# Kernel optimization log

Measured on AMD Instinct MI355X. Metric: run time of the kernel, lower is better.

## Reference

```python
import jax, jax.numpy as jnp
import numpy as np

N_NODES = 100000
N_EDGES = 1280000
IN_DIM = 64
OUT_DIM = 64


def setup_inputs() -> dict:
    key = jax.random.key(0)
    k1, k2, k3, k4, k5 = jax.random.split(key, 5)
    features = jax.random.normal(k1, (N_NODES, IN_DIM), dtype=jnp.float32)
    w = jax.random.uniform(k2, (N_EDGES,), dtype=jnp.float32)
    # torch nn.Linear weight is [out, in]; we store it as [in, out] so h @ W
    W = jax.random.normal(k3, (IN_DIM, OUT_DIM), dtype=jnp.float32) * (1.0 / np.sqrt(IN_DIM))
    src = jax.random.randint(k4, (N_EDGES,), 0, N_NODES, dtype=jnp.int64 if jax.config.jax_enable_x64 else jnp.int32)
    dst = jax.random.randint(k5, (N_EDGES,), 0, N_NODES, dtype=jnp.int64 if jax.config.jax_enable_x64 else jnp.int32)
    return {"features": features, "w": w, "W": W, "src": src, "dst": dst}


def reference(features, w, W, src, dst):
    num_nodes = features.shape[0]
    # u_mul_e: per-edge message = h[src] * w  (edge-weighted SpMM gather-multiply)
    msg = features[src] * w[:, None]                     # [E, in_dim]
    # fn.sum('m','h'): scatter-add messages to destination nodes
    agg = jax.ops.segment_sum(msg, dst, num_segments=num_nodes)  # [N, in_dim]
    # D_in = 1 / clamp(in_degree, min=1)
    deg = jax.ops.segment_sum(jnp.ones_like(w), dst, num_segments=num_nodes)
    d_in = 1.0 / jnp.maximum(deg, 1.0)                   # [N]
    h = agg * d_in[:, None]
    # linear (bias=False), activation None, batch_norm False, dropout 0
    return h @ W                                         # [N, out_dim]
```

## Files before the change

kernel.cpp:

```cpp
#include <hip/hip_runtime.h>

#define N_NODES 100000
#define N_EDGES 1280000
#define DIM 64
#define NBINS 391
#define CAP 3712
#define EPB 4096
#define NFB 313
#define CONVB 512
#define WSCALE (1.0f / 32767.0f)

__device__ __forceinline__ unsigned bf16_rne(float x) {
    unsigned u = __float_as_uint(x);
    return (u + 0x7fffu + ((u >> 16) & 1u)) >> 16;
}
__device__ __forceinline__ float rl_f(float v, int l) {
    return __int_as_float(__builtin_amdgcn_readlane(__float_as_int(v), l));
}
__device__ __forceinline__ float bf_lo(unsigned q) { return __uint_as_float(q << 16); }
__device__ __forceinline__ float bf_hi(unsigned q) { return __uint_as_float(q & 0xffff0000u); }

__global__ __launch_bounds__(256) void k_fill_conv(
    const int* __restrict__ src, const float* __restrict__ w,
    const int* __restrict__ dst, int* __restrict__ cursor,
    uint2* __restrict__ binned,
    const float* __restrict__ feat, const float* __restrict__ W,
    unsigned short* __restrict__ fW) {
    __shared__ int h[NBINS];
    __shared__ int base_[NBINS];
    int t = threadIdx.x;

    if (blockIdx.x < NFB) {
        for (int i = t; i < NBINS; i += 256) h[i] = 0;
        __syncthreads();
        int eb = blockIdx.x * EPB;
        int d[16], sv[16];
        unsigned wq[16];
        #pragma unroll
        for (int j = 0; j < 16; ++j) {
            int e = eb + j * 256 + t;
            if (e < N_EDGES) {
                d[j] = dst[e];
                sv[j] = src[e];
                wq[j] = (unsigned)(w[e] * 32767.0f + 0.5f);
                atomicAdd(&h[d[j] >> 8], 1);
            } else d[j] = -1;
        }
        __syncthreads();
        for (int i = t; i < NBINS; i += 256) {
            int c = h[i];
            base_[i] = c ? atomicAdd(&cursor[i], c) : 0;
            h[i] = 0;
        }
        __syncthreads();
        #pragma unroll
        for (int j = 0; j < 16; ++j) {
            if (d[j] >= 0) {
                int bin = d[j] >> 8;
                int pos = base_[bin] + atomicAdd(&h[bin], 1);
                binned[bin * CAP + pos] =
                    make_uint2((unsigned)sv[j] | ((unsigned)(d[j] & 255) << 17), wq[j]);
            }
        }
    } else {
        int lane = t & 63;
        float wcol[DIM];
        #pragma unroll
        for (int k = 0; k < DIM; ++k) wcol[k] = W[k * DIM + lane];
        int wave = ((blockIdx.x - NFB) * 256 + t) >> 6;
        int nw = CONVB * 4;
        for (int n0 = wave; n0 < N_NODES; n0 += 2 * nw) {
            int n1 = n0 + nw;
            float ha = feat[n0 * DIM + lane];
            float hb = (n1 < N_NODES) ? feat[n1 * DIM + lane] : 0.f;
            float a0 = 0, a1 = 0, a2 = 0, a3 = 0, b0 = 0, b1 = 0, b2 = 0, b3 = 0;
            #pragma unroll
            for (int k = 0; k < DIM; k += 4) {
                a0 = fmaf(rl_f(ha, k + 0), wcol[k + 0], a0);
                a1 = fmaf(rl_f(ha, k + 1), wcol[k + 1], a1);
                a2 = fmaf(rl_f(ha, k + 2), wcol[k + 2], a2);
                a3 = fmaf(rl_f(ha, k + 3), wcol[k + 3], a3);
                b0 = fmaf(rl_f(hb, k + 0), wcol[k + 0], b0);
                b1 = fmaf(rl_f(hb, k + 1), wcol[k + 1], b1);
                b2 = fmaf(rl_f(hb, k + 2), wcol[k + 2], b2);
                b3 = fmaf(rl_f(hb, k + 3), wcol[k + 3], b3);
            }
            fW[n0 * DIM + lane] = (unsigned short)bf16_rne((a0 + a1) + (a2 + a3));
            if (n1 < N_NODES)
                fW[n1 * DIM + lane] = (unsigned short)bf16_rne((b0 + b1) + (b2 + b3));
        }
    }
}

__global__ __launch_bounds__(256) void k_sortbin(const uint2* __restrict__ binned,
                                                 const int* __restrict__ cursor,
                                                 unsigned* __restrict__ csrp,
                                                 int* __restrict__ offs,
                                                 int* __restrict__ cnt) {
    __shared__ int h[256];
    __shared__ int excl[256];
    __shared__ unsigned stage[CAP];
    int b = blockIdx.x, t = threadIdx.x;
    int total = cursor[b];
    int segbase = b * CAP;
    h[t] = 0;
    __syncthreads();
    for (int i = t; i < total; i += 256)
        atomicAdd(&h[(binned[segbase + i].x >> 17) & 255], 1);
    __syncthreads();
    int v = h[t];
    excl[t] = v;
    __syncthreads();
    for (int off = 1; off < 256; off <<= 1) {
        int add = (t >= off) ? excl[t - off] : 0;
        __syncthreads();
        excl[t] += add;
        __syncthreads();
    }
    int ex = excl[t] - v;
    excl[t] = ex;
    int node = (b << 8) + t;
    if (node < N_NODES) { cnt[node] = v; offs[node] = segbase + ex; }
    h[t] = 0;
    __syncthreads();
    for (int i = t; i < total; i += 256) {
        uint2 e = binned[segbase + i];
        int o = (e.x >> 17) & 255;
        int pos = excl[o] + atomicAdd(&h[o], 1);
        if (pos < CAP) stage[pos] = (e.x & 0x1ffffu) | (e.y << 17);
    }
    __syncthreads();
    for (int i = t; i < total; i += 256)
        csrp[segbase + i] = stage[i];
}

__global__ __launch_bounds__(256) void k_gather(const uint4* __restrict__ fW4,
                                                const unsigned* __restrict__ csrp,
                                                const int* __restrict__ offs,
                                                const int* __restrict__ cnt,
                                                float* __restrict__ out) {
    int lane = threadIdx.x & 63;
    int g = lane >> 3, s = lane & 7;
    int wave = (blockIdx.x * 256 + threadIdx.x) >> 6;
    int nw = gridDim.x * 4;

    for (int node = wave; node < N_NODES; node += nw) {
        int start = offs[node];
        int c = cnt[node];
        int end = start + c;
        float a[8] = {0, 0, 0, 0, 0, 0, 0, 0};
        for (int i = start; i < end; i += 16) {
            int i0 = i + g, i1 = i + 8 + g;
            unsigned p0 = csrp[(i0 < end) ? i0 : start];
            unsigned p1 = csrp[(i1 < end) ? i1 : start];
            float w0 = (i0 < end) ? (float)(p0 >> 17) * WSCALE : 0.f;
            float w1 = (i1 < end) ? (float)(p1 >> 17) * WSCALE : 0.f;
            uint4 q0 = fW4[((p0 & 0x1ffffu) << 3) + s];
            uint4 q1 = fW4[((p1 & 0x1ffffu) << 3) + s];
            a[0] = fmaf(bf_lo(q0.x), w0, a[0]); a[1] = fmaf(bf_hi(q0.x), w0, a[1]);
            a[2] = fmaf(bf_lo(q0.y), w0, a[2]); a[3] = fmaf(bf_hi(q0.y), w0, a[3]);
            a[4] = fmaf(bf_lo(q0.z), w0, a[4]); a[5] = fmaf(bf_hi(q0.z), w0, a[5]);
            a[6] = fmaf(bf_lo(q0.w), w0, a[6]); a[7] = fmaf(bf_hi(q0.w), w0, a[7]);
            a[0] = fmaf(bf_lo(q1.x), w1, a[0]); a[1] = fmaf(bf_hi(q1.x), w1, a[1]);
            a[2] = fmaf(bf_lo(q1.y), w1, a[2]); a[3] = fmaf(bf_hi(q1.y), w1, a[3]);
            a[4] = fmaf(bf_lo(q1.z), w1, a[4]); a[5] = fmaf(bf_hi(q1.z), w1, a[5]);
            a[6] = fmaf(bf_lo(q1.w), w1, a[6]); a[7] = fmaf(bf_hi(q1.w), w1, a[7]);
        }
        #pragma unroll
        for (int j = 0; j < 8; ++j) {
            a[j] += __shfl_xor(a[j], 8, 64);
            a[j] += __shfl_xor(a[j], 16, 64);
            a[j] += __shfl_xor(a[j], 32, 64);
        }
        float dinv = 1.0f / fmaxf((float)c, 1.0f);
        if (g == 0) {
            float4 o0, o1;
            o0.x = a[0] * dinv; o0.y = a[1] * dinv; o0.z = a[2] * dinv; o0.w = a[3] * dinv;
            o1.x = a[4] * dinv; o1.y = a[5] * dinv; o1.z = a[6] * dinv; o1.w = a[7] * dinv;
            ((float4*)out)[node * 16 + s * 2 + 0] = o0;
            ((float4*)out)[node * 16 + s * 2 + 1] = o1;
        }
    }
}

extern "C" void kernel_launch(void* const* d_in, const int* in_sizes, int n_in,
                              void* d_out, int out_size, void* d_ws, size_t ws_size,
                              hipStream_t stream) {
    const float* feat = (const float*)d_in[0];
    const float* w    = (const float*)d_in[1];
    const float* W    = (const float*)d_in[2];
    const int*   src  = (const int*)d_in[3];
    const int*   dst  = (const int*)d_in[4];
    float* out = (float*)d_out;

    unsigned short* fW = (unsigned short*)d_ws;
    uint2* binned  = (uint2*)(fW + (size_t)N_NODES * DIM);
    unsigned* csrp = (unsigned*)(binned + (size_t)NBINS * CAP);
    int* offs      = (int*)(csrp + (size_t)NBINS * CAP);
    int* cnt       = offs + N_NODES;
    int* cursor    = cnt + N_NODES;

    hipMemsetAsync(cursor, 0, NBINS * sizeof(int), stream);

    k_fill_conv<<<NFB + CONVB, 256, 0, stream>>>(src, w, dst, cursor, binned,
                                                 feat, W, fW);
    k_sortbin<<<NBINS, 256, 0, stream>>>(binned, cursor, csrp, offs, cnt);
    k_gather<<<4096, 256, 0, stream>>>((const uint4*)fW, csrp, offs, cnt, out);
}
```

Baseline: 168.9 us.

## Replace readlane-based feature transform with LDS-tiled 4x4 register-blocked GEMM

The per-node feature×W projection now stages W and 64-node feature tiles in shared memory, and each thread computes a 4x4 output block from float4 LDS reads. Previously each wave ran 64 serial readlane+FMA steps per node. The new version raises arithmetic intensity and writes bf16 results with vectorized ushort4 stores. In exchange it adds about 33KB of LDS per block through a union with the binning histogram, which may lower occupancy for the co-scheduled fill blocks.

```diff
diff --git a/kernel.cpp b/kernel.cpp
--- a/kernel.cpp
+++ b/kernel.cpp
@@ -8,14 +8,13 @@
 #define EPB 4096
 #define NFB 313
 #define CONVB 512
+#define NTILES 1563
+#define FPAD 68
 #define WSCALE (1.0f / 32767.0f)
 
 __device__ __forceinline__ unsigned bf16_rne(float x) {
     unsigned u = __float_as_uint(x);
     return (u + 0x7fffu + ((u >> 16) & 1u)) >> 16;
-}
-__device__ __forceinline__ float rl_f(float v, int l) {
-    return __int_as_float(__builtin_amdgcn_readlane(__float_as_int(v), l));
 }
 __device__ __forceinline__ float bf_lo(unsigned q) { return __uint_as_float(q << 16); }
 __device__ __forceinline__ float bf_hi(unsigned q) { return __uint_as_float(q & 0xffff0000u); }
@@ -26,12 +25,15 @@
     uint2* __restrict__ binned,
     const float* __restrict__ feat, const float* __restrict__ W,
     unsigned short* __restrict__ fW) {
-    __shared__ int h[NBINS];
-    __shared__ int base_[NBINS];
+    __shared__ union U {
+        struct { int h[NBINS]; int base_[NBINS]; } fill;
+        struct { float w[DIM * DIM]; float f[64 * FPAD]; } conv;
+        __device__ U() {}
+    } sm;
     int t = threadIdx.x;
 
     if (blockIdx.x < NFB) {
-        for (int i = t; i < NBINS; i += 256) h[i] = 0;
+        for (int i = t; i < NBINS; i += 256) sm.fill.h[i] = 0;
         __syncthreads();
         int eb = blockIdx.x * EPB;
         int d[16], sv[16];
@@ -43,51 +45,83 @@
                 d[j] = dst[e];
                 sv[j] = src[e];
                 wq[j] = (unsigned)(w[e] * 32767.0f + 0.5f);
-                atomicAdd(&h[d[j] >> 8], 1);
+                atomicAdd(&sm.fill.h[d[j] >> 8], 1);
             } else d[j] = -1;
         }
         __syncthreads();
         for (int i = t; i < NBINS; i += 256) {
-            int c = h[i];
-            base_[i] = c ? atomicAdd(&cursor[i], c) : 0;
-            h[i] = 0;
+            int c = sm.fill.h[i];
+            sm.fill.base_[i] = c ? atomicAdd(&cursor[i], c) : 0;
+            sm.fill.h[i] = 0;
         }
         __syncthreads();
         #pragma unroll
         for (int j = 0; j < 16; ++j) {
             if (d[j] >= 0) {
                 int bin = d[j] >> 8;
-                int pos = base_[bin] + atomicAdd(&h[bin], 1);
+                int pos = sm.fill.base_[bin] + atomicAdd(&sm.fill.h[bin], 1);
                 binned[bin * CAP + pos] =
                     make_uint2((unsigned)sv[j] | ((unsigned)(d[j] & 255) << 17), wq[j]);
             }
         }
     } else {
-        int lane = t & 63;
-        float wcol[DIM];
-        #pragma unroll
-        for (int k = 0; k < DIM; ++k) wcol[k] = W[k * DIM + lane];
-        int wave = ((blockIdx.x - NFB) * 256 + t) >> 6;
-        int nw = CONVB * 4;
-        for (int n0 = wave; n0 < N_NODES; n0 += 2 * nw) {
-            int n1 = n0 + nw;
-            float ha = feat[n0 * DIM + lane];
-            float hb = (n1 < N_NODES) ? feat[n1 * DIM + lane] : 0.f;
-            float a0 = 0, a1 = 0, a2 = 0, a3 = 0, b0 = 0, b1 = 0, b2 = 0, b3 = 0;
+        #pragma unroll
+        for (int i = 0; i < DIM * DIM / 256; ++i)
+            sm.conv.w[t + i * 256] = W[t + i * 256];
+        const float4* lds_w4 = (const float4*)sm.conv.w;
+        float4* lds_f4 = (float4*)sm.conv.f;
+        int tx = t & 15, ny = t >> 4;
+        int rr = t >> 2, seg = t & 3;
+
+        for (int tb = blockIdx.x - NFB; tb < NTILES; tb += CONVB) {
+            int nb = tb * 64;
+            __syncthreads();
             #pragma unroll
-            for (int k = 0; k < DIM; k += 4) {
-                a0 = fmaf(rl_f(ha, k + 0), wcol[k + 0], a0);
-                a1 = fmaf(rl_f(ha, k + 1), wcol[k + 1], a1);
-                a2 = fmaf(rl_f(ha, k + 2), wcol[k + 2], a2);
-                a3 = fmaf(rl_f(ha, k + 3), wcol[k + 3], a3);
-                b0 = fmaf(rl_f(hb, k + 0), wcol[k + 0], b0);
-                b1 = fmaf(rl_f(hb, k + 1), wcol[k + 1], b1);
-                b2 = fmaf(rl_f(hb, k + 2), wcol[k + 2], b2);
-                b3 = fmaf(rl_f(hb, k + 3), wcol[k + 3], b3);
-            }
-            fW[n0 * DIM + lane] = (unsigned short)bf16_rne((a0 + a1) + (a2 + a3));
-            if (n1 < N_NODES)
-                fW[n1 * DIM + lane] = (unsigned short)bf16_rne((b0 + b1) + (b2 + b3));
+            for (int q = 0; q < 4; ++q) {
+                float4 v = (nb + rr < N_NODES)
+                           ? ((const float4*)feat)[(size_t)(nb + rr) * 16 + seg * 4 + q]
+                           : make_float4(0.f, 0.f, 0.f, 0.f);
+                lds_f4[(rr * FPAD + seg * 16 + q * 4) >> 2] = v;
+            }
+            __syncthreads();
+            float acc[4][4];
+            #pragma unroll
+            for (int i = 0; i < 4; ++i)
+                #pragma unroll
+                for (int j = 0; j < 4; ++j) acc[i][j] = 0.f;
+            for (int k0 = 0; k0 < DIM; k0 += 4) {
+                float4 hv[4], wv[4];
+                #pragma unroll
+                for (int i = 0; i < 4; ++i)
+                    hv[i] = lds_f4[((ny * 4 + i) * FPAD + k0) >> 2];
+                #pragma unroll
+                for (int j = 0; j < 4; ++j)
+                    wv[j] = lds_w4[((k0 + j) * DIM + tx * 4) >> 2];
+                #pragma unroll
+                for (int i = 0; i < 4; ++i) {
+                    const float* hp = (const float*)&hv[i];
+                    #pragma unroll
+                    for (int kk = 0; kk < 4; ++kk) {
+                        float hk = hp[kk];
+                        acc[i][0] = fmaf(hk, ((const float*)&wv[kk])[0], acc[i][0]);
+                        acc[i][1] = fmaf(hk, ((const float*)&wv[kk])[1], acc[i][1]);
+                        acc[i][2] = fmaf(hk, ((const float*)&wv[kk])[2], acc[i][2]);
+                        acc[i][3] = fmaf(hk, ((const float*)&wv[kk])[3], acc[i][3]);
+                    }
+                }
+            }
+            #pragma unroll
+            for (int i = 0; i < 4; ++i) {
+                int node = nb + ny * 4 + i;
+                if (node < N_NODES) {
+                    ushort4 o;
+                    o.x = (unsigned short)bf16_rne(acc[i][0]);
+                    o.y = (unsigned short)bf16_rne(acc[i][1]);
+                    o.z = (unsigned short)bf16_rne(acc[i][2]);
+                    o.w = (unsigned short)bf16_rne(acc[i][3]);
+                    *(ushort4*)(fW + (size_t)node * DIM + tx * 4) = o;
+                }
+            }
         }
     }
 }
```

After: 156.1 us. 7.5% less time.
